# Kernel tuning notes

Hardware: AMD Instinct MI355X
Metric: run time of the kernel (lower is better)

## Reference

```python
import jax, jax.numpy as jnp
import numpy as np

B, L, D, H, NB = 256, 200, 128, 4, 2
ITEMS = 50000
EPS = 1e-8
C = 0.001
REG = 0.0001


def _ln(x, g, b):
    m = x.mean(-1, keepdims=True)
    v = ((x - m) ** 2).mean(-1, keepdims=True)
    return (x - m) / jnp.sqrt(v + EPS) * g + b


def _mha(q_in, kv_in, in_w, in_b, out_w, out_b, mask):
    # q_in, kv_in: (B, L, D); torch MultiheadAttention math (batch-layout equivalent)
    Wq, Wk, Wv = jnp.split(in_w, 3, axis=0)
    bq, bk, bv = jnp.split(in_b, 3, axis=0)
    hd = D // H
    heads = lambda x: x.reshape(B, L, H, hd).transpose(0, 2, 1, 3)
    q = heads(q_in @ Wq.T + bq)
    k = heads(kv_in @ Wk.T + bk)
    v = heads(kv_in @ Wv.T + bv)
    scores = jnp.einsum('bhqd,bhkd->bhqk', q, k) * (1.0 / np.sqrt(hd))
    scores = jnp.where(mask, -jnp.inf, scores)
    a = jax.nn.softmax(scores, axis=-1)
    o = jnp.einsum('bhqk,bhkd->bhqd', a, v).transpose(0, 2, 1, 3).reshape(B, L, D)
    return o @ out_w.T + out_b


def _log2feats(log_seqs, item_emb, pos_emb, blocks):
    seqs = item_emb[log_seqs]                                   # (B,L,D)
    poss = jnp.arange(1, L + 1)[None, :] * (log_seqs != 0)      # 0 at padding
    seqs = seqs + pos_emb[poss]
    mask = ~jnp.tril(jnp.ones((L, L), dtype=bool))              # causal
    for i in range(NB):
        (ln1_g, ln1_b, in_w, in_b, out_w, out_b,
         ln2_g, ln2_b, c1_w, c1_b, c2_w, c2_b) = [p[i] for p in blocks]
        Q = _ln(seqs, ln1_g, ln1_b)
        seqs = Q + _mha(Q, seqs, in_w, in_b, out_w, out_b, mask)  # residual on Q (as in source)
        seqs = _ln(seqs, ln2_g, ln2_b)
        # PointWiseFeedForward: conv1d k=1 == linear over feature dim, residual add
        seqs = seqs + (jax.nn.relu(seqs @ c1_w.T + c1_b) @ c2_w.T + c2_b)
    return seqs


def setup_inputs() -> dict:
    key = jax.random.key(0)
    ks = jax.random.split(key, 20)
    inp = {
        'user_ids': jax.random.randint(ks[0], (B,), 0, 10000),
        'log_seqs': jax.random.randint(ks[1], (B, L), 0, ITEMS + 1),
        'pos_seqs': jax.random.randint(ks[2], (B, L), 0, ITEMS + 1),
        'item_emb': (jax.random.normal(ks[3], (ITEMS + 1, D)) * 0.02).at[0].set(0.0),
        'pos_emb': (jax.random.normal(ks[4], (L + 1, D)) * 0.02).at[0].set(0.0),
        'pred_w': jax.random.normal(ks[5], (1, D)) * 0.05,
        'ln1_g': jnp.ones((NB, D)), 'ln1_b': jnp.zeros((NB, D)),
        'in_w': jax.random.normal(ks[6], (NB, 3 * D, D)) * 0.05,
        'in_b': jnp.zeros((NB, 3 * D)),
        'out_w': jax.random.normal(ks[7], (NB, D, D)) * 0.05,
        'out_b': jnp.zeros((NB, D)),
        'ln2_g': jnp.ones((NB, D)), 'ln2_b': jnp.zeros((NB, D)),
        'c1_w': jax.random.normal(ks[8], (NB, D, D)) * 0.05,
        'c1_b': jnp.zeros((NB, D)),
        'c2_w': jax.random.normal(ks[9], (NB, D, D)) * 0.05,
        'c2_b': jnp.zeros((NB, D)),
    }
    return inp


def reference(user_ids, log_seqs, pos_seqs, item_emb, pos_emb, pred_w,
              ln1_g, ln1_b, in_w, in_b, out_w, out_b, ln2_g, ln2_b,
              c1_w, c1_b, c2_w, c2_b):
    blocks = (ln1_g, ln1_b, in_w, in_b, out_w, out_b, ln2_g, ln2_b, c1_w, c1_b, c2_w, c2_b)
    F = _log2feats(log_seqs, item_emb, pos_emb, blocks)          # (B,L,D)
    # left: FF = sum_s F F^T (per batch), EE = E^T E over full catalog, hh = w^T w
    FF = jnp.einsum('bsd,bse->bde', F, F)                        # (B,D,D)
    EE = item_emb.T @ item_emb                                   # (D,D)
    hh = pred_w.T @ pred_w                                       # (D,D)
    left = jnp.einsum('bde,ef,fg->b', FF, C * EE, hh)            # sum of FF @ cEE @ hh
    # right: R_hat = h^T (F * q_i)
    pos_e = item_emb[pos_seqs]                                   # (B,L,D)
    R = jnp.einsum('d,bsd->bs', pred_w[0], F * pos_e)
    right = ((1.0 - C) * R ** 2 - 2.0 * R).sum(axis=-1)
    reg = jnp.sqrt((item_emb ** 2).sum())                        # Frobenius norm
    loss = left + right + REG * reg
    return loss.mean()
```

## Files before the change

kernel.cpp:

```cpp
#include <hip/hip_runtime.h>
#include <math.h>

#define B_ 256
#define L_ 200
#define D_ 128
#define H_ 4
#define HD_ 32
#define NB_ 2
#define NROWS (B_ * L_)
#define NITEMS 50001
#define EPS_ 1e-8f
#define C_ 0.001f
#define REG_ 0.0001f

typedef __bf16 bf16x8 __attribute__((ext_vector_type(8)));
typedef short  short8 __attribute__((ext_vector_type(8)));
typedef float  f32x4  __attribute__((ext_vector_type(4)));

static __device__ __forceinline__ unsigned short f2bf(float f) {
  unsigned u = __builtin_bit_cast(unsigned, f);
  unsigned r = (u + 0x7FFFu + ((u >> 16) & 1u)) >> 16;
  return (unsigned short)r;
}
static __device__ __forceinline__ float bf2f(unsigned short s) {
  return __builtin_bit_cast(float, (unsigned)s << 16);
}

__global__ __launch_bounds__(256) void k_embed(const int* __restrict__ logs,
                                               const float* __restrict__ item_emb,
                                               const float* __restrict__ pos_emb,
                                               float* __restrict__ X) {
  int gid = blockIdx.x * 256 + threadIdx.x;
  if (gid >= NROWS * 32) return;
  int row = gid >> 5;
  int c4  = (gid & 31) << 2;
  int it  = logs[row];
  int l   = row % L_;
  int pos = (it != 0) ? (l + 1) : 0;
  float4 e = *(const float4*)(item_emb + (size_t)it * D_ + c4);
  float4 p = *(const float4*)(pos_emb + (size_t)pos * D_ + c4);
  float4 o; o.x = e.x + p.x; o.y = e.y + p.y; o.z = e.z + p.z; o.w = e.w + p.w;
  *(float4*)(X + (size_t)row * D_ + c4) = o;
}

__global__ __launch_bounds__(256) void k_ln(const float* __restrict__ in,
                                            const float* __restrict__ g,
                                            const float* __restrict__ bb,
                                            float* __restrict__ out) {
  int wid = threadIdx.x >> 6, lane = threadIdx.x & 63;
  int row = blockIdx.x * 4 + wid;
  float2 x = *(const float2*)(in + (size_t)row * D_ + lane * 2);
  float s = x.x + x.y;
#pragma unroll
  for (int o = 1; o < 64; o <<= 1) s += __shfl_xor(s, o, 64);
  float m = s * (1.f / D_);
  float d0 = x.x - m, d1 = x.y - m;
  float ss = d0 * d0 + d1 * d1;
#pragma unroll
  for (int o = 1; o < 64; o <<= 1) ss += __shfl_xor(ss, o, 64);
  float rs = 1.f / sqrtf(ss * (1.f / D_) + EPS_);
  float2 gv = *(const float2*)(g + lane * 2);
  float2 bv = *(const float2*)(bb + lane * 2);
  float2 o2; o2.x = d0 * rs * gv.x + bv.x; o2.y = d1 * rs * gv.y + bv.y;
  *(float2*)(out + (size_t)row * D_ + lane * 2) = o2;
}

__global__ __launch_bounds__(256) void k_gemm_mfma(const float* __restrict__ A, int lda,
                                                   const float* __restrict__ W,
                                                   const float* __restrict__ bias,
                                                   const float* __restrict__ Res,
                                                   float* __restrict__ Cmat, int ldc,
                                                   int col0, int epi) {
  W    += (size_t)blockIdx.y * 128 * 128;
  bias += blockIdx.y * 128;
  col0 += blockIdx.y * 128;
  __shared__ float As[64][132];
  const int tid  = threadIdx.x;
  const int bm   = blockIdx.x * 64;
  const int lane = tid & 63, wid = tid >> 6;
  const int n0   = wid * 32;
  const int fr   = lane & 15;
  const int fg   = lane >> 4;

  bf16x8 bh[2][4], bl[2][4];
#pragma unroll
  for (int f = 0; f < 2; f++)
#pragma unroll
    for (int ks = 0; ks < 4; ks++) {
      const float* wp = W + (size_t)(n0 + f * 16 + fr) * 128 + ks * 32 + fg * 8;
      float4 w0 = *(const float4*)wp;
      float4 w1 = *(const float4*)(wp + 4);
      float wf[8] = {w0.x, w0.y, w0.z, w0.w, w1.x, w1.y, w1.z, w1.w};
      short8 h, l2;
#pragma unroll
      for (int j = 0; j < 8; j++) {
        unsigned short hb = f2bf(wf[j]);
        h[j]  = (short)hb;
        l2[j] = (short)f2bf(wf[j] - bf2f(hb));
      }
      bh[f][ks] = __builtin_bit_cast(bf16x8, h);
      bl[f][ks] = __builtin_bit_cast(bf16x8, l2);
    }

#pragma unroll
  for (int i = 0; i < 8; i++) {
    int flat = i * 1024 + tid * 4;
    int r = flat >> 7, c = flat & 127;
    float4 v = *(const float4*)(A + (size_t)(bm + r) * lda + c);
    *(float4*)&As[r][c] = v;
  }
  __syncthreads();

  f32x4 acc[4][2];
#pragma unroll
  for (int m = 0; m < 4; m++)
#pragma unroll
    for (int f = 0; f < 2; f++) acc[m][f] = (f32x4)0.f;

#pragma unroll
  for (int m = 0; m < 4; m++) {
#pragma unroll
    for (int ks = 0; ks < 4; ks++) {
      const float* ap = &As[m * 16 + fr][ks * 32 + fg * 8];
      float4 a0 = *(const float4*)ap;
      float4 a1 = *(const float4*)(ap + 4);
      float af[8] = {a0.x, a0.y, a0.z, a0.w, a1.x, a1.y, a1.z, a1.w};
      short8 h, l2;
#pragma unroll
      for (int j = 0; j < 8; j++) {
        unsigned short hb = f2bf(af[j]);
        h[j]  = (short)hb;
        l2[j] = (short)f2bf(af[j] - bf2f(hb));
      }
      bf16x8 ah = __builtin_bit_cast(bf16x8, h);
      bf16x8 al = __builtin_bit_cast(bf16x8, l2);
#pragma unroll
      for (int f = 0; f < 2; f++) {
        acc[m][f] = __builtin_amdgcn_mfma_f32_16x16x32_bf16(ah, bl[f][ks], acc[m][f], 0, 0, 0);
        acc[m][f] = __builtin_amdgcn_mfma_f32_16x16x32_bf16(al, bh[f][ks], acc[m][f], 0, 0, 0);
        acc[m][f] = __builtin_amdgcn_mfma_f32_16x16x32_bf16(ah, bh[f][ks], acc[m][f], 0, 0, 0);
      }
    }
  }

#pragma unroll
  for (int f = 0; f < 2; f++) {
    int n = n0 + f * 16 + fr;
    float bv = bias[n];
#pragma unroll
    for (int m = 0; m < 4; m++) {
#pragma unroll
      for (int i = 0; i < 4; i++) {
        int row = bm + m * 16 + fg * 4 + i;
        float v = acc[m][f][i] + bv;
        if (epi == 2)      v = fmaxf(v, 0.f);
        else if (epi == 1) v += Res[(size_t)row * D_ + n];
        Cmat[(size_t)row * ldc + col0 + n] = v;
      }
    }
  }
}

__global__ __launch_bounds__(256) void k_attn(const float* __restrict__ qkv,
                                              float* __restrict__ Oq) {
  __shared__ float ks[L_][HD_];
  __shared__ float vs[L_][HD_];
  int b = blockIdx.x >> 2;
  int h = blockIdx.x & 3;
  int tid = threadIdx.x;
  for (int idx = tid; idx < L_ * HD_; idx += 256) {
    int j = idx >> 5, d = idx & 31;
    size_t base = ((size_t)(b * L_ + j)) * 384 + 128 + h * HD_ + d;
    ks[j][d] = qkv[base];
    vs[j][d] = qkv[base + 128];
  }
  __syncthreads();
  int t = tid;
  if (t >= L_) return;
  float q[HD_];
  const float* qp = qkv + ((size_t)(b * L_ + t)) * 384 + h * HD_;
#pragma unroll
  for (int d4 = 0; d4 < HD_; d4 += 4) {
    float4 v = *(const float4*)(qp + d4);
    q[d4] = v.x; q[d4 + 1] = v.y; q[d4 + 2] = v.z; q[d4 + 3] = v.w;
  }
  float o[HD_];
#pragma unroll
  for (int d = 0; d < HD_; d++) o[d] = 0.f;
  float mrun = -INFINITY, lrun = 0.f;
  const float scale = 0.17677669529663687f;
  for (int j = 0; j <= t; j++) {
    float s = 0.f;
#pragma unroll
    for (int d = 0; d < HD_; d++) s += q[d] * ks[j][d];
    s *= scale;
    float mn = fmaxf(mrun, s);
    float corr = __expf(mrun - mn);
    float p = __expf(s - mn);
    lrun = lrun * corr + p;
#pragma unroll
    for (int d = 0; d < HD_; d++) o[d] = o[d] * corr + p * vs[j][d];
    mrun = mn;
  }
  float inv = 1.f / lrun;
  float* op = Oq + ((size_t)(b * L_ + t)) * 384 + h * HD_;
#pragma unroll
  for (int d4 = 0; d4 < HD_; d4 += 4) {
    float4 v;
    v.x = o[d4] * inv; v.y = o[d4 + 1] * inv;
    v.z = o[d4 + 2] * inv; v.w = o[d4 + 3] * inv;
    *(float4*)(op + d4) = v;
  }
}

__global__ void k_zero(float* __restrict__ w_raw, float* __restrict__ reg_sq) {
  int t = threadIdx.x;
  if (t < 128) w_raw[t] = 0.f;
  if (t == 128) reg_sq[0] = 0.f;
}

__global__ __launch_bounds__(256) void k_wreg(const float* __restrict__ item_emb,
                                              const float* __restrict__ pred_w,
                                              float* __restrict__ w_raw,
                                              float* __restrict__ reg_sq) {
  int gw = (blockIdx.x * 256 + threadIdx.x) >> 6;
  int lane = threadIdx.x & 63;
  float2 p2 = *(const float2*)(pred_w + lane * 2);
  float ax = 0.f, ay = 0.f, ssq = 0.f;
  for (int r = gw; r < NITEMS; r += 1024) {
    float2 e = *(const float2*)(item_emb + (size_t)r * D_ + lane * 2);
    float dp = e.x * p2.x + e.y * p2.y;
#pragma unroll
    for (int o = 1; o < 64; o <<= 1) dp += __shfl_xor(dp, o, 64);
    ax += e.x * dp; ay += e.y * dp;
    ssq += e.x * e.x + e.y * e.y;
  }
  atomicAdd(&w_raw[lane * 2 + 0], ax);
  atomicAdd(&w_raw[lane * 2 + 1], ay);
#pragma unroll
  for (int o = 1; o < 64; o <<= 1) ssq += __shfl_xor(ssq, o, 64);
  if (lane == 0) atomicAdd(reg_sq, ssq);
}

__global__ void k_scale(const float* __restrict__ pred_w,
                        const float* __restrict__ w_raw,
                        const float* __restrict__ reg_sq,
                        float* __restrict__ wt, float* __restrict__ out) {
  int t = threadIdx.x;
  __shared__ float sp[128];
  sp[t] = pred_w[t];
  __syncthreads();
  float S = 0.f;
  for (int i = 0; i < 128; i++) S += sp[i];
  wt[t] = C_ * S * w_raw[t];
  if (t == 0) out[0] = REG_ * sqrtf(reg_sq[0]);
}

__global__ __launch_bounds__(256) void k_final(const float* __restrict__ F,
                                               const int* __restrict__ pos_seqs,
                                               const float* __restrict__ item_emb,
                                               const float* __restrict__ pred_w,
                                               const float* __restrict__ wt,
                                               float* __restrict__ out) {
  int b = blockIdx.x;
  int wid = threadIdx.x >> 6, lane = threadIdx.x & 63;
  float2 wt2 = *(const float2*)(wt + lane * 2);
  float2 p2  = *(const float2*)(pred_w + lane * 2);
  float acc = 0.f;
  for (int s = wid; s < L_; s += 4) {
    float2 f = *(const float2*)(F + ((size_t)(b * L_ + s)) * D_ + lane * 2);
    int pi = pos_seqs[b * L_ + s];
    float2 pe = *(const float2*)(item_emb + (size_t)pi * D_ + lane * 2);
    float rsum = f.x + f.y;
    float dw = f.x * wt2.x + f.y * wt2.y;
    float rr = p2.x * f.x * pe.x + p2.y * f.y * pe.y;
#pragma unroll
    for (int o = 1; o < 64; o <<= 1) {
      rsum += __shfl_xor(rsum, o, 64);
      dw   += __shfl_xor(dw, o, 64);
      rr   += __shfl_xor(rr, o, 64);
    }
    acc += rsum * dw + (1.f - C_) * rr * rr - 2.f * rr;
  }
  if (lane == 0) atomicAdd(out, acc * (1.f / B_));
}

extern "C" void kernel_launch(void* const* d_in, const int* in_sizes, int n_in,
                              void* d_out, int out_size, void* d_ws, size_t ws_size,
                              hipStream_t stream) {
  const int*   log_seqs = (const int*)d_in[1];
  const int*   pos_seqs = (const int*)d_in[2];
  const float* item_emb = (const float*)d_in[3];
  const float* pos_emb  = (const float*)d_in[4];
  const float* pred_w   = (const float*)d_in[5];
  const float* ln1_g = (const float*)d_in[6];
  const float* ln1_b = (const float*)d_in[7];
  const float* in_w  = (const float*)d_in[8];
  const float* in_b  = (const float*)d_in[9];
  const float* out_w = (const float*)d_in[10];
  const float* out_b = (const float*)d_in[11];
  const float* ln2_g = (const float*)d_in[12];
  const float* ln2_b = (const float*)d_in[13];
  const float* c1_w  = (const float*)d_in[14];
  const float* c1_b  = (const float*)d_in[15];
  const float* c2_w  = (const float*)d_in[16];
  const float* c2_b  = (const float*)d_in[17];
  float* out = (float*)d_out;

  char* ws = (char*)d_ws;
  const size_t UNIT = (size_t)NROWS * D_ * sizeof(float);
  float* X     = (float*)ws; ws += UNIT;
  float* QB    = (float*)ws; ws += UNIT;
  float* QKV   = (float*)ws; ws += 3 * UNIT;
  float* w_raw = (float*)ws; ws += 512;
  float* wt    = (float*)ws; ws += 512;
  float* reg_sq= (float*)ws; ws += 512;
  if (ws_size < 5 * UNIT + 4096) return;

  k_zero<<<1, 256, 0, stream>>>(w_raw, reg_sq);
  k_embed<<<(NROWS * 32) / 256, 256, 0, stream>>>(log_seqs, item_emb, pos_emb, X);

  for (int i = 0; i < NB_; i++) {
    const float* iw = in_w + (size_t)i * 384 * 128;
    const float* ib = in_b + (size_t)i * 384;
    k_ln<<<NROWS / 4, 256, 0, stream>>>(X, ln1_g + i * 128, ln1_b + i * 128, QB);
    k_gemm_mfma<<<dim3(NROWS / 64, 1), 256, 0, stream>>>(QB, 128, iw, ib, nullptr, QKV, 384, 0, 0);
    k_gemm_mfma<<<dim3(NROWS / 64, 2), 256, 0, stream>>>(X, 128, iw + 128 * 128, ib + 128,
                                                         nullptr, QKV, 384, 128, 0);
    k_attn<<<B_ * H_, 256, 0, stream>>>(QKV, QKV);
    k_gemm_mfma<<<dim3(NROWS / 64, 1), 256, 0, stream>>>(QKV, 384, out_w + (size_t)i * 128 * 128,
                                                         out_b + i * 128, QB, X, 128, 0, 1);
    k_ln<<<NROWS / 4, 256, 0, stream>>>(X, ln2_g + i * 128, ln2_b + i * 128, QB);
    k_gemm_mfma<<<dim3(NROWS / 64, 1), 256, 0, stream>>>(QB, 128, c1_w + (size_t)i * 128 * 128,
                                                         c1_b + i * 128, nullptr, QKV, 128, 0, 2);
    k_gemm_mfma<<<dim3(NROWS / 64, 1), 256, 0, stream>>>(QKV, 128, c2_w + (size_t)i * 128 * 128,
                                                         c2_b + i * 128, QB, X, 128, 0, 1);
  }

  k_wreg<<<256, 256, 0, stream>>>(item_emb, pred_w, w_raw, reg_sq);
  k_scale<<<1, 128, 0, stream>>>(pred_w, w_raw, reg_sq, wt, out);
  k_final<<<B_, 256, 0, stream>>>(X, pos_seqs, item_emb, pred_w, wt, out);
}
```

Before: 830.1 us.

## Pre-split weights into bf16 hi/lo once and split A tiles at LDS staging

```diff
diff --git a/kernel.cpp b/kernel.cpp
--- a/kernel.cpp
+++ b/kernel.cpp
@@ -16,14 +16,46 @@
 typedef __bf16 bf16x8 __attribute__((ext_vector_type(8)));
 typedef short  short8 __attribute__((ext_vector_type(8)));
 typedef float  f32x4  __attribute__((ext_vector_type(4)));
-
-static __device__ __forceinline__ unsigned short f2bf(float f) {
+typedef unsigned short us4 __attribute__((ext_vector_type(4)));
+
+static __device__ __forceinline__ void split2(float f, unsigned short& h, unsigned short& l) {
   unsigned u = __builtin_bit_cast(unsigned, f);
-  unsigned r = (u + 0x7FFFu + ((u >> 16) & 1u)) >> 16;
-  return (unsigned short)r;
-}
-static __device__ __forceinline__ float bf2f(unsigned short s) {
-  return __builtin_bit_cast(float, (unsigned)s << 16);
+  unsigned hb = (u + 0x7FFFu + ((u >> 16) & 1u)) >> 16;
+  float fl = f - __builtin_bit_cast(float, hb << 16);
+  h = (unsigned short)hb;
+  l = (unsigned short)(__builtin_bit_cast(unsigned, fl) >> 16);
+}
+
+static __device__ __forceinline__ bf16x8 pack8(const unsigned short* s) {
+  short8 v;
+#pragma unroll
+  for (int j = 0; j < 8; ++j) v[j] = (short)s[j];
+  return __builtin_bit_cast(bf16x8, v);
+}
+
+__global__ __launch_bounds__(256) void k_convw(const float* __restrict__ in_w,
+                                               const float* __restrict__ out_w,
+                                               const float* __restrict__ c1_w,
+                                               const float* __restrict__ c2_w,
+                                               unsigned short* __restrict__ Wh,
+                                               unsigned short* __restrict__ Wl) {
+  int i = (blockIdx.x * 256 + threadIdx.x) * 4;
+  if (i >= 196608) return;
+  const float* s; int j;
+  if (i < 98304)       { s = in_w;  j = i; }
+  else if (i < 131072) { s = out_w; j = i - 98304; }
+  else if (i < 163840) { s = c1_w;  j = i - 131072; }
+  else                 { s = c2_w;  j = i - 163840; }
+  float4 v = *(const float4*)(s + j);
+  float vf[4] = {v.x, v.y, v.z, v.w};
+  us4 hv, lv;
+#pragma unroll
+  for (int t = 0; t < 4; ++t) {
+    unsigned short h, l; split2(vf[t], h, l);
+    hv[t] = h; lv[t] = l;
+  }
+  *(us4*)(Wh + i) = hv;
+  *(us4*)(Wl + i) = lv;
 }
 
 __global__ __launch_bounds__(256) void k_embed(const int* __restrict__ logs,
@@ -65,16 +97,18 @@
   *(float2*)(out + (size_t)row * D_ + lane * 2) = o2;
 }
 
-__global__ __launch_bounds__(256) void k_gemm_mfma(const float* __restrict__ A, int lda,
-                                                   const float* __restrict__ W,
-                                                   const float* __restrict__ bias,
-                                                   const float* __restrict__ Res,
-                                                   float* __restrict__ Cmat, int ldc,
-                                                   int col0, int epi) {
-  W    += (size_t)blockIdx.y * 128 * 128;
+__global__ __launch_bounds__(256) void k_gemm2(const float* __restrict__ A, int lda,
+                                               const unsigned short* __restrict__ Wh,
+                                               const unsigned short* __restrict__ Wl,
+                                               const float* __restrict__ bias,
+                                               const float* __restrict__ Res,
+                                               float* __restrict__ Cmat, int ldc,
+                                               int col0, int epi) {
+  Wh   += (size_t)blockIdx.y * 128 * 128;
+  Wl   += (size_t)blockIdx.y * 128 * 128;
   bias += blockIdx.y * 128;
   col0 += blockIdx.y * 128;
-  __shared__ float As[64][132];
+  __shared__ unsigned short Ah[64][136], Al[64][136];
   const int tid  = threadIdx.x;
   const int bm   = blockIdx.x * 64;
   const int lane = tid & 63, wid = tid >> 6;
@@ -82,32 +116,30 @@
   const int fr   = lane & 15;
   const int fg   = lane >> 4;
 
-  bf16x8 bh[2][4], bl[2][4];
+  bf16x8 wh[2][4], wl[2][4];
 #pragma unroll
   for (int f = 0; f < 2; f++)
 #pragma unroll
     for (int ks = 0; ks < 4; ks++) {
-      const float* wp = W + (size_t)(n0 + f * 16 + fr) * 128 + ks * 32 + fg * 8;
-      float4 w0 = *(const float4*)wp;
-      float4 w1 = *(const float4*)(wp + 4);
-      float wf[8] = {w0.x, w0.y, w0.z, w0.w, w1.x, w1.y, w1.z, w1.w};
-      short8 h, l2;
-#pragma unroll
-      for (int j = 0; j < 8; j++) {
-        unsigned short hb = f2bf(wf[j]);
-        h[j]  = (short)hb;
-        l2[j] = (short)f2bf(wf[j] - bf2f(hb));
-      }
-      bh[f][ks] = __builtin_bit_cast(bf16x8, h);
-      bl[f][ks] = __builtin_bit_cast(bf16x8, l2);
+      const unsigned short* p = Wh + (size_t)(n0 + f * 16 + fr) * 128 + ks * 32 + fg * 8;
+      const unsigned short* q = Wl + (size_t)(n0 + f * 16 + fr) * 128 + ks * 32 + fg * 8;
+      wh[f][ks] = __builtin_bit_cast(bf16x8, *(const short8*)p);
+      wl[f][ks] = __builtin_bit_cast(bf16x8, *(const short8*)q);
     }
 
 #pragma unroll
-  for (int i = 0; i < 8; i++) {
-    int flat = i * 1024 + tid * 4;
+  for (int it = 0; it < 4; ++it) {
+    int flat = it * 2048 + tid * 8;
     int r = flat >> 7, c = flat & 127;
-    float4 v = *(const float4*)(A + (size_t)(bm + r) * lda + c);
-    *(float4*)&As[r][c] = v;
+    const float* ap = A + (size_t)(bm + r) * lda + c;
+    float4 a0 = *(const float4*)ap;
+    float4 a1 = *(const float4*)(ap + 4);
+    float af[8] = {a0.x, a0.y, a0.z, a0.w, a1.x, a1.y, a1.z, a1.w};
+    unsigned short hh[8], ll[8];
+#pragma unroll
+    for (int j = 0; j < 8; ++j) split2(af[j], hh[j], ll[j]);
+    *(short8*)&Ah[r][c] = __builtin_bit_cast(short8, pack8(hh));
+    *(short8*)&Al[r][c] = __builtin_bit_cast(short8, pack8(ll));
   }
   __syncthreads();
 
@@ -115,30 +147,19 @@
 #pragma unroll
   for (int m = 0; m < 4; m++)
 #pragma unroll
-    for (int f = 0; f < 2; f++) acc[m][f] = (f32x4)0.f;
+    for (int f = 0; f < 2; f++) acc[m][f] = (f32x4){0.f, 0.f, 0.f, 0.f};
 
 #pragma unroll
   for (int m = 0; m < 4; m++) {
 #pragma unroll
     for (int ks = 0; ks < 4; ks++) {
-      const float* ap = &As[m * 16 + fr][ks * 32 + fg * 8];
-      float4 a0 = *(const float4*)ap;
-      float4 a1 = *(const float4*)(ap + 4);
-      float af[8] = {a0.x, a0.y, a0.z, a0.w, a1.x, a1.y, a1.z, a1.w};
-      short8 h, l2;
-#pragma unroll
-      for (int j = 0; j < 8; j++) {
-        unsigned short hb = f2bf(af[j]);
-        h[j]  = (short)hb;
-        l2[j] = (short)f2bf(af[j] - bf2f(hb));
-      }
-      bf16x8 ah = __builtin_bit_cast(bf16x8, h);
-      bf16x8 al = __builtin_bit_cast(bf16x8, l2);
+      bf16x8 ah = *(const bf16x8*)&Ah[m * 16 + fr][ks * 32 + fg * 8];
+      bf16x8 al = *(const bf16x8*)&Al[m * 16 + fr][ks * 32 + fg * 8];
 #pragma unroll
       for (int f = 0; f < 2; f++) {
-        acc[m][f] = __builtin_amdgcn_mfma_f32_16x16x32_bf16(ah, bl[f][ks], acc[m][f], 0, 0, 0);
-        acc[m][f] = __builtin_amdgcn_mfma_f32_16x16x32_bf16(al, bh[f][ks], acc[m][f], 0, 0, 0);
-        acc[m][f] = __builtin_amdgcn_mfma_f32_16x16x32_bf16(ah, bh[f][ks], acc[m][f], 0, 0, 0);
+        acc[m][f] = __builtin_amdgcn_mfma_f32_16x16x32_bf16(ah, wl[f][ks], acc[m][f], 0, 0, 0);
+        acc[m][f] = __builtin_amdgcn_mfma_f32_16x16x32_bf16(al, wh[f][ks], acc[m][f], 0, 0, 0);
+        acc[m][f] = __builtin_amdgcn_mfma_f32_16x16x32_bf16(ah, wh[f][ks], acc[m][f], 0, 0, 0);
       }
     }
   }
@@ -312,29 +333,40 @@
   float* X     = (float*)ws; ws += UNIT;
   float* QB    = (float*)ws; ws += UNIT;
   float* QKV   = (float*)ws; ws += 3 * UNIT;
+  unsigned short* WH = (unsigned short*)ws; ws += 196608 * 2;
+  unsigned short* WL = (unsigned short*)ws; ws += 196608 * 2;
   float* w_raw = (float*)ws; ws += 512;
   float* wt    = (float*)ws; ws += 512;
   float* reg_sq= (float*)ws; ws += 512;
-  if (ws_size < 5 * UNIT + 4096) return;
+  if (ws_size < 5 * UNIT + 4 * 196608 + 4096) return;
+
+  const size_t OFF_OUT = 98304, OFF_C1 = 131072, OFF_C2 = 163840;
 
   k_zero<<<1, 256, 0, stream>>>(w_raw, reg_sq);
+  k_convw<<<192, 256, 0, stream>>>(in_w, out_w, c1_w, c2_w, WH, WL);
   k_embed<<<(NROWS * 32) / 256, 256, 0, stream>>>(log_seqs, item_emb, pos_emb, X);
 
   for (int i = 0; i < NB_; i++) {
-    const float* iw = in_w + (size_t)i * 384 * 128;
+    const size_t iwo = (size_t)i * 384 * 128;
+    const size_t sqo = (size_t)i * 128 * 128;
     const float* ib = in_b + (size_t)i * 384;
     k_ln<<<NROWS / 4, 256, 0, stream>>>(X, ln1_g + i * 128, ln1_b + i * 128, QB);
-    k_gemm_mfma<<<dim3(NROWS / 64, 1), 256, 0, stream>>>(QB, 128, iw, ib, nullptr, QKV, 384, 0, 0);
-    k_gemm_mfma<<<dim3(NROWS / 64, 2), 256, 0, stream>>>(X, 128, iw + 128 * 128, ib + 128,
-                                                         nullptr, QKV, 384, 128, 0);
+    k_gemm2<<<dim3(NROWS / 64, 1), 256, 0, stream>>>(QB, 128, WH + iwo, WL + iwo,
+                                                     ib, nullptr, QKV, 384, 0, 0);
+    k_gemm2<<<dim3(NROWS / 64, 2), 256, 0, stream>>>(X, 128, WH + iwo + 128 * 128,
+                                                     WL + iwo + 128 * 128,
+                                                     ib + 128, nullptr, QKV, 384, 128, 0);
     k_attn<<<B_ * H_, 256, 0, stream>>>(QKV, QKV);
-    k_gemm_mfma<<<dim3(NROWS / 64, 1), 256, 0, stream>>>(QKV, 384, out_w + (size_t)i * 128 * 128,
-                                                         out_b + i * 128, QB, X, 128, 0, 1);
+    k_gemm2<<<dim3(NROWS / 64, 1), 256, 0, stream>>>(QKV, 384, WH + OFF_OUT + sqo,
+                                                     WL + OFF_OUT + sqo,
+                                                     out_b + i * 128, QB, X, 128, 0, 1);
     k_ln<<<NROWS / 4, 256, 0, stream>>>(X, ln2_g + i * 128, ln2_b + i * 128, QB);
-    k_gemm_mfma<<<dim3(NROWS / 64, 1), 256, 0, stream>>>(QB, 128, c1_w + (size_t)i * 128 * 128,
-                                                         c1_b + i * 128, nullptr, QKV, 128, 0, 2);
-    k_gemm_mfma<<<dim3(NROWS / 64, 1), 256, 0, stream>>>(QKV, 128, c2_w + (size_t)i * 128 * 128,
-                                                         c2_b + i * 128, QB, X, 128, 0, 1);
+    k_gemm2<<<dim3(NROWS / 64, 1), 256, 0, stream>>>(QB, 128, WH + OFF_C1 + sqo,
+                                                     WL + OFF_C1 + sqo,
+                                                     c1_b + i * 128, nullptr, QKV, 128, 0, 2);
+    k_gemm2<<<dim3(NROWS / 64, 1), 256, 0, stream>>>(QKV, 128, WH + OFF_C2 + sqo,
+                                                     WL + OFF_C2 + sqo,
+                                                     c2_b + i * 128, QB, X, 128, 0, 1);
   }
 
   k_wreg<<<256, 256, 0, stream>>>(item_emb, pred_w, w_raw, reg_sq);
```

Measured after the change: 786.9 us. -5.2%, faster.
